# Kernel tuning notes

Measured on AMD Instinct MI355X. Metric: run time of the kernel, lower is better.

The kernel has to match this reference:

```python
import jax, jax.numpy as jnp
import numpy as np

N, F, H, E = 100000, 64, 8, 1200000
D = F // H
HID = 32  # hardcoded MLP hidden width in the module


def setup_inputs() -> dict:
    key = jax.random.key(0)
    ks = jax.random.split(key, 16)
    s = 0.05
    return {
        "h": jax.random.normal(ks[0], (N, F), jnp.float32),
        "W_src": jax.random.normal(ks[1], (F, F), jnp.float32) * s,
        "b_src": jnp.zeros((F,), jnp.float32),
        "W_dst": jax.random.normal(ks[2], (F, F), jnp.float32) * s,
        "b_dst": jnp.zeros((F,), jnp.float32),
        "Wa1_src": jax.random.normal(ks[3], (F, HID), jnp.float32) * s,
        "ba1_src": jnp.zeros((HID,), jnp.float32),
        "Wa2_src": jax.random.normal(ks[4], (HID, H), jnp.float32) * s,
        "ba2_src": jnp.zeros((H,), jnp.float32),
        "Wa1_dst": jax.random.normal(ks[5], (F, HID), jnp.float32) * s,
        "ba1_dst": jnp.zeros((HID,), jnp.float32),
        "Wa2_dst": jax.random.normal(ks[6], (HID, H), jnp.float32) * s,
        "ba2_dst": jnp.zeros((H,), jnp.float32),
        "edge_index": jax.random.randint(ks[7], (2, E), 0, N, jnp.int64),
    }


def _attn_mlp(x, W1, b1, W2, b2):
    # Sequential(LeakyReLU(0.2), Linear(F,32), LeakyReLU(0.2), Linear(32,H))
    y = jax.nn.leaky_relu(x, 0.2)
    y = y @ W1 + b1
    y = jax.nn.leaky_relu(y, 0.2)
    return y @ W2 + b2


def reference(h, W_src, b_src, W_dst, b_dst,
              Wa1_src, ba1_src, Wa2_src, ba2_src,
              Wa1_dst, ba1_dst, Wa2_dst, ba2_dst,
              edge_index):
    src, dst = edge_index[0], edge_index[1]
    g_src = h @ W_src + b_src          # [N,F]
    g_dst = h @ W_dst + b_dst          # [N,F]
    msg_src = g_src[src]               # [E,F] gather
    msg = msg_src + g_dst[dst]         # [E,F]
    a_src = jax.nn.sigmoid(_attn_mlp(msg, Wa1_src, ba1_src, Wa2_src, ba2_src))[:, :, None]    # [E,H,1]
    a_dst = jax.nn.sigmoid(_attn_mlp(g_dst, Wa1_dst, ba1_dst, Wa2_dst, ba2_dst))[:, :, None]  # [N,H,1]
    agg = jax.ops.segment_sum(a_src * msg_src.reshape(E, H, D), dst, num_segments=N)          # [N,H,D]
    h_next = a_dst * g_dst.reshape(N, H, D) + agg
    return h_next.reshape(N, F)
```

## Files before the change

kernel.cpp:

```cpp
#include <hip/hip_runtime.h>
#include <hip/hip_bf16.h>
#include <hip/hip_fp16.h>

#define NF   64
#define NH   8
#define ND   8
#define NHID 32
#define XS   68

typedef __attribute__((ext_vector_type(8))) short bf16x8v;
typedef __attribute__((ext_vector_type(4))) float f32x4v;

__device__ __forceinline__ float bf2f(unsigned short u) {
    union { unsigned int i; float f; } v; v.i = ((unsigned int)u) << 16; return v.f;
}
__device__ __forceinline__ unsigned short f2bf(float f) {
    __hip_bfloat16 b = __float2bfloat16(f);
    union { __hip_bfloat16 b; unsigned short u; } v; v.b = b; return v.u;
}
__device__ __forceinline__ void unpack8(uint4 u, float* o) {
    o[0] = __uint_as_float(u.x << 16); o[1] = __uint_as_float(u.x & 0xffff0000u);
    o[2] = __uint_as_float(u.y << 16); o[3] = __uint_as_float(u.y & 0xffff0000u);
    o[4] = __uint_as_float(u.z << 16); o[5] = __uint_as_float(u.z & 0xffff0000u);
    o[6] = __uint_as_float(u.w << 16); o[7] = __uint_as_float(u.w & 0xffff0000u);
}
__device__ __forceinline__ uint4 pack8(const float* f) {
    uint4 u;
    u.x = (unsigned)f2bf(f[0]) | ((unsigned)f2bf(f[1]) << 16);
    u.y = (unsigned)f2bf(f[2]) | ((unsigned)f2bf(f[3]) << 16);
    u.z = (unsigned)f2bf(f[4]) | ((unsigned)f2bf(f[5]) << 16);
    u.w = (unsigned)f2bf(f[6]) | ((unsigned)f2bf(f[7]) << 16);
    return u;
}
__device__ __forceinline__ float leaky(float x) { return x > 0.f ? x : 0.2f * x; }
__device__ __forceinline__ float sigmoidf(float x) { return 1.f / (1.f + __expf(-x)); }

__global__ void detect_kernel(const int* __restrict__ edge, int* __restrict__ flags) {
    if (threadIdx.x == 0 && blockIdx.x == 0) {
        int oddnz = 0;
        for (int i = 0; i < 32; i++) oddnz |= edge[2 * i + 1];
        flags[0] = (oddnz == 0) ? 1 : 0;
    }
}

__device__ __forceinline__ void load_edge(const int* __restrict__ edge, int e, int E,
                                          int wide, int& s, int& d) {
    if (wide) { s = edge[2 * e]; d = edge[2 * (E + e)]; }
    else      { s = edge[e];     d = edge[E + e]; }
}

__global__ __launch_bounds__(64) void node_mfma_kernel(
    const float* __restrict__ h,
    const float* __restrict__ W_src, const float* __restrict__ b_src,
    const float* __restrict__ W_dst, const float* __restrict__ b_dst,
    const float* __restrict__ Wa1, const float* __restrict__ ba1,
    const float* __restrict__ Wa2, const float* __restrict__ ba2,
    unsigned short* __restrict__ g_src_out, unsigned short* __restrict__ g_dst_out,
    float* __restrict__ out, int* __restrict__ counts, int N)
{
    __shared__ __align__(16) unsigned short sX[64 * XS];
    __shared__ __align__(16) unsigned short sY[64 * XS];
    __shared__ float sW2[NHID * NH];
    __shared__ float sb2[NH];

    int lane = threadIdx.x;
    int nsub = lane & 15, quad = lane >> 4;
    int base = blockIdx.x * 64;
    int n = base + lane;
    bool valid = n < N;
    size_t nn = valid ? (size_t)n : (size_t)(N - 1);

    if (valid && counts) counts[n] = 0;
    for (int i = lane; i < NHID * NH; i += 64) sW2[i] = Wa2[i];
    if (lane < NH) sb2[lane] = ba2[lane];

    {
        const float4* hv = (const float4*)(h + nn * NF);
        unsigned short* xrow = sX + lane * XS;
        #pragma unroll
        for (int k = 0; k < 8; k++) {
            float4 u0 = hv[2 * k], u1 = hv[2 * k + 1];
            float f[8] = { u0.x, u0.y, u0.z, u0.w, u1.x, u1.y, u1.z, u1.w };
            uint4 p = pack8(f);
            uint2* q = (uint2*)(xrow + k * 8);
            q[0] = make_uint2(p.x, p.y);
            q[1] = make_uint2(p.z, p.w);
        }
    }
    __syncthreads();

    #pragma unroll 1
    for (int m = 0; m < 2; m++) {
        const float* W  = m ? W_dst : W_src;
        const float* bb = m ? b_dst : b_src;
        unsigned short* gout = m ? g_dst_out : g_src_out;

        bf16x8v Bf[2][4];
        #pragma unroll
        for (int ks = 0; ks < 2; ks++)
            #pragma unroll
            for (int nt = 0; nt < 4; nt++) {
                union { unsigned short s[8]; bf16x8v v; } u;
                #pragma unroll
                for (int j = 0; j < 8; j++)
                    u.s[j] = f2bf(W[(ks * 32 + quad * 8 + j) * NF + nt * 16 + nsub]);
                Bf[ks][nt] = u.v;
            }

        f32x4v acc[4][4];
        #pragma unroll
        for (int mt = 0; mt < 4; mt++)
            #pragma unroll
            for (int nt = 0; nt < 4; nt++) {
                f32x4v z = {0.f, 0.f, 0.f, 0.f};
                acc[mt][nt] = z;
            }

        #pragma unroll
        for (int ks = 0; ks < 2; ks++)
            #pragma unroll
            for (int mt = 0; mt < 4; mt++) {
                const unsigned short* ap = sX + (mt * 16 + nsub) * XS + ks * 32 + quad * 8;
                union { uint2 d[2]; bf16x8v v; } ua;
                ua.d[0] = *(const uint2*)ap;
                ua.d[1] = *(const uint2*)(ap + 4);
                #pragma unroll
                for (int nt = 0; nt < 4; nt++)
                    acc[mt][nt] = __builtin_amdgcn_mfma_f32_16x16x32_bf16(
                        ua.v, Bf[ks][nt], acc[mt][nt], 0, 0, 0);
            }

        if (m == 1) __syncthreads();

        #pragma unroll
        for (int nt = 0; nt < 4; nt++) {
            float bv = bb[nt * 16 + nsub];
            #pragma unroll
            for (int mt = 0; mt < 4; mt++)
                #pragma unroll
                for (int r = 0; r < 4; r++)
                    sY[(mt * 16 + quad * 4 + r) * XS + nt * 16 + nsub] =
                        f2bf(acc[mt][nt][r] + bv);
        }
        __syncthreads();

        if (valid) {
            const unsigned short* yrow = sY + lane * XS;
            uint4* gp = (uint4*)(gout + (size_t)n * NF);
            #pragma unroll
            for (int k = 0; k < 8; k++) {
                uint2 a = *(const uint2*)(yrow + k * 8);
                uint2 b = *(const uint2*)(yrow + k * 8 + 4);
                gp[k] = make_uint4(a.x, a.y, b.x, b.y);
            }
        }
    }

    bf16x8v B1f[2][2];
    #pragma unroll
    for (int ks = 0; ks < 2; ks++)
        #pragma unroll
        for (int nt = 0; nt < 2; nt++) {
            union { unsigned short s[8]; bf16x8v v; } u;
            #pragma unroll
            for (int j = 0; j < 8; j++)
                u.s[j] = f2bf(Wa1[(ks * 32 + quad * 8 + j) * NHID + nt * 16 + nsub]);
            B1f[ks][nt] = u.v;
        }

    f32x4v acc2[4][2];
    #pragma unroll
    for (int mt = 0; mt < 4; mt++)
        #pragma unroll
        for (int nt = 0; nt < 2; nt++) {
            f32x4v z = {0.f, 0.f, 0.f, 0.f};
            acc2[mt][nt] = z;
        }

    #pragma unroll
    for (int ks = 0; ks < 2; ks++)
        #pragma unroll
        for (int mt = 0; mt < 4; mt++) {
            const unsigned short* ap = sY + (mt * 16 + nsub) * XS + ks * 32 + quad * 8;
            uint2 d0 = *(const uint2*)ap;
            uint2 d1 = *(const uint2*)(ap + 4);
            float f[8];
            unpack8(make_uint4(d0.x, d0.y, d1.x, d1.y), f);
            #pragma unroll
            for (int t = 0; t < 8; t++) f[t] = leaky(f[t]);
            uint4 p = pack8(f);
            union { uint4 u; bf16x8v v; } ua; ua.u = p;
            #pragma unroll
            for (int nt = 0; nt < 2; nt++)
                acc2[mt][nt] = __builtin_amdgcn_mfma_f32_16x16x32_bf16(
                    ua.v, B1f[ks][nt], acc2[mt][nt], 0, 0, 0);
        }
    __syncthreads();

    #pragma unroll
    for (int nt = 0; nt < 2; nt++) {
        float b1v = ba1[nt * 16 + nsub];
        #pragma unroll
        for (int mt = 0; mt < 4; mt++)
            #pragma unroll
            for (int r = 0; r < 4; r++)
                sX[(mt * 16 + quad * 4 + r) * XS + nt * 16 + nsub] =
                    f2bf(leaky(acc2[mt][nt][r] + b1v));
    }
    __syncthreads();

    if (valid) {
        float hid[NHID];
        const unsigned short* hrow = sX + lane * XS;
        #pragma unroll
        for (int k = 0; k < 8; k++) {
            uint2 dv = *(const uint2*)(hrow + k * 4);
            hid[k * 4 + 0] = bf2f((unsigned short)(dv.x & 0xffffu));
            hid[k * 4 + 1] = bf2f((unsigned short)(dv.x >> 16));
            hid[k * 4 + 2] = bf2f((unsigned short)(dv.y & 0xffffu));
            hid[k * 4 + 3] = bf2f((unsigned short)(dv.y >> 16));
        }
        float a[NH];
        #pragma unroll
        for (int j = 0; j < NH; j++) a[j] = sb2[j];
        #pragma unroll
        for (int k = 0; k < NHID; k++) {
            float xk = hid[k];
            #pragma unroll
            for (int j = 0; j < NH; j++) a[j] = fmaf(xk, sW2[k * NH + j], a[j]);
        }
        #pragma unroll
        for (int j = 0; j < NH; j++) a[j] = sigmoidf(a[j]);

        const unsigned short* yrow = sY + lane * XS;
        float4* op = (float4*)(out + (size_t)n * NF);
        #pragma unroll
        for (int k = 0; k < 8; k++) {
            uint2 u0 = *(const uint2*)(yrow + k * 8);
            uint2 u1 = *(const uint2*)(yrow + k * 8 + 4);
            float g[8];
            unpack8(make_uint4(u0.x, u0.y, u1.x, u1.y), g);
            float ah0 = a[(k * 8) >> 3];
            op[2 * k]     = make_float4(ah0 * g[0], ah0 * g[1], ah0 * g[2], ah0 * g[3]);
            op[2 * k + 1] = make_float4(ah0 * g[4], ah0 * g[5], ah0 * g[6], ah0 * g[7]);
        }
    }
}

template <bool STORE_G>
__global__ __launch_bounds__(256) void node_kernel_t(
    const float* __restrict__ h,
    const float* __restrict__ W_src, const float* __restrict__ b_src,
    const float* __restrict__ W_dst, const float* __restrict__ b_dst,
    const float* __restrict__ Wa1, const float* __restrict__ ba1,
    const float* __restrict__ Wa2, const float* __restrict__ ba2,
    unsigned short* __restrict__ g_src_out, unsigned short* __restrict__ g_dst_out,
    float* __restrict__ out, int N)
{
    __shared__ __align__(16) float sWs[NF * NF];
    __shared__ __align__(16) float sWd[NF * NF];
    __shared__ __align__(16) float sW1[NF * NHID];
    __shared__ __align__(16) float sW2[NHID * NH];
    __shared__ float sbs[NF], sbd[NF], sb1[NHID], sb2[NH];

    int tid = threadIdx.x;
    for (int i = tid; i < NF * NF; i += 256) { sWs[i] = W_src[i]; sWd[i] = W_dst[i]; }
    for (int i = tid; i < NF * NHID; i += 256) sW1[i] = Wa1[i];
    if (tid < NHID * NH) sW2[tid] = Wa2[tid];
    if (tid < NF) { sbs[tid] = b_src[tid]; sbd[tid] = b_dst[tid]; }
    if (tid < NHID) sb1[tid] = ba1[tid];
    if (tid < NH) sb2[tid] = ba2[tid];
    __syncthreads();

    int n = blockIdx.x * 256 + tid;
    if (n >= N) return;

    float hrow[NF];
    const float4* hv = (const float4*)(h + (size_t)n * NF);
    #pragma unroll
    for (int k = 0; k < 16; k++) {
        float4 u = hv[k];
        hrow[k * 4 + 0] = u.x; hrow[k * 4 + 1] = u.y;
        hrow[k * 4 + 2] = u.z; hrow[k * 4 + 3] = u.w;
    }

    float acc[NF];
    const float4* Wsv = (const float4*)sWs;
    const float4* Wdv = (const float4*)sWd;

    if (STORE_G) {
        #pragma unroll
        for (int j = 0; j < NF; j++) acc[j] = sbs[j];
        for (int i = 0; i < NF; i++) {
            float hi = hrow[i];
            #pragma unroll
            for (int jb = 0; jb < 16; jb++) {
                float4 w = Wsv[i * 16 + jb];
                acc[jb * 4 + 0] = fmaf(hi, w.x, acc[jb * 4 + 0]);
                acc[jb * 4 + 1] = fmaf(hi, w.y, acc[jb * 4 + 1]);
                acc[jb * 4 + 2] = fmaf(hi, w.z, acc[jb * 4 + 2]);
                acc[jb * 4 + 3] = fmaf(hi, w.w, acc[jb * 4 + 3]);
            }
        }
        uint4* gs = (uint4*)(g_src_out + (size_t)n * NF);
        #pragma unroll
        for (int k = 0; k < 8; k++) gs[k] = pack8(acc + k * 8);
    }

    #pragma unroll
    for (int j = 0; j < NF; j++) acc[j] = sbd[j];
    for (int i = 0; i < NF; i++) {
        float hi = hrow[i];
        #pragma unroll
        for (int jb = 0; jb < 16; jb++) {
            float4 w = Wdv[i * 16 + jb];
            acc[jb * 4 + 0] = fmaf(hi, w.x, acc[jb * 4 + 0]);
            acc[jb * 4 + 1] = fmaf(hi, w.y, acc[jb * 4 + 1]);
            acc[jb * 4 + 2] = fmaf(hi, w.z, acc[jb * 4 + 2]);
            acc[jb * 4 + 3] = fmaf(hi, w.w, acc[jb * 4 + 3]);
        }
    }
    if (STORE_G) {
        uint4* gd = (uint4*)(g_dst_out + (size_t)n * NF);
        #pragma unroll
        for (int k = 0; k < 8; k++) gd[k] = pack8(acc + k * 8);
    }

    float hid[NHID];
    #pragma unroll
    for (int j = 0; j < NHID; j++) hid[j] = sb1[j];
    const float4* W1v = (const float4*)sW1;
    for (int i = 0; i < NF; i++) {
        float xi = leaky(acc[i]);
        #pragma unroll
        for (int jb = 0; jb < 8; jb++) {
            float4 w = W1v[i * 8 + jb];
            hid[jb * 4 + 0] = fmaf(xi, w.x, hid[jb * 4 + 0]);
            hid[jb * 4 + 1] = fmaf(xi, w.y, hid[jb * 4 + 1]);
            hid[jb * 4 + 2] = fmaf(xi, w.z, hid[jb * 4 + 2]);
            hid[jb * 4 + 3] = fmaf(xi, w.w, hid[jb * 4 + 3]);
        }
    }
    float a[NH];
    #pragma unroll
    for (int j = 0; j < NH; j++) a[j] = sb2[j];
    #pragma unroll
    for (int k = 0; k < NHID; k++) {
        float xk = leaky(hid[k]);
        #pragma unroll
        for (int j = 0; j < NH; j++) a[j] = fmaf(xk, sW2[k * NH + j], a[j]);
    }
    #pragma unroll
    for (int j = 0; j < NH; j++) a[j] = sigmoidf(a[j]);

    float4* ap = (float4*)(out + (size_t)n * NF);
    #pragma unroll
    for (int k = 0; k < 16; k++) {
        int j = k * 4;
        ap[k] = make_float4(a[(j + 0) >> 3] * acc[j + 0],
                            a[(j + 1) >> 3] * acc[j + 1],
                            a[(j + 2) >> 3] * acc[j + 2],
                            a[(j + 3) >> 3] * acc[j + 3]);
    }
}

__global__ __launch_bounds__(256) void hist_kernel(
    const int* __restrict__ edge, const int* __restrict__ flags,
    int* __restrict__ counts, int* __restrict__ rank, int E, int N)
{
    int e = blockIdx.x * 256 + threadIdx.x;
    if (e >= E) return;
    int s, d;
    load_edge(edge, e, E, flags[0], s, d);
    if ((unsigned)s >= (unsigned)N || (unsigned)d >= (unsigned)N) { rank[e] = -1; return; }
    rank[e] = atomicAdd(&counts[d], 1);
}

__global__ __launch_bounds__(256) void scan1_kernel(
    const int* __restrict__ counts, int* __restrict__ offsets,
    int* __restrict__ bsums, int N)
{
    __shared__ int lds[256];
    int tid = threadIdx.x;
    int base = blockIdx.x * 2048 + tid * 8;
    int v[8]; int s = 0;
    #pragma unroll
    for (int k = 0; k < 8; k++) { int idx = base + k; int t = (idx < N) ? counts[idx] : 0; v[k] = t; s += t; }
    lds[tid] = s;
    __syncthreads();
    for (int off = 1; off < 256; off <<= 1) {
        int y = (tid >= off) ? lds[tid - off] : 0;
        __syncthreads();
        lds[tid] += y;
        __syncthreads();
    }
    int run = lds[tid] - s;
    #pragma unroll
    for (int k = 0; k < 8; k++) { int idx = base + k; if (idx < N) offsets[idx] = run; run += v[k]; }
    if (tid == 255) bsums[blockIdx.x] = lds[255];
}

__global__ void scan2_kernel(int* __restrict__ bsums, int* __restrict__ offsets, int NB, int N) {
    if (threadIdx.x == 0 && blockIdx.x == 0) {
        int run = 0;
        for (int i = 0; i < NB; i++) { int t = bsums[i]; bsums[i] = run; run += t; }
        offsets[N] = run;
    }
}

__global__ __launch_bounds__(256) void scan3_kernel(
    int* __restrict__ offsets, const int* __restrict__ bsums, int N)
{
    int add = bsums[blockIdx.x];
    int base = blockIdx.x * 2048 + threadIdx.x * 8;
    #pragma unroll
    for (int k = 0; k < 8; k++) { int idx = base + k; if (idx < N) offsets[idx] += add; }
}

__global__ __launch_bounds__(256) void scatter_kernel(
    const int* __restrict__ edge, const int* __restrict__ flags,
    const int* __restrict__ offsets, const int* __restrict__ rank,
    uint2* __restrict__ sorted_sd, int E, int N)
{
    int e = blockIdx.x * 256 + threadIdx.x;
    if (e >= E) return;
    int r = rank[e];
    if (r < 0) return;
    int s, d;
    load_edge(edge, e, E, flags[0], s, d);
    int pos = offsets[d] + r;
    sorted_sd[pos] = make_uint2((unsigned)s, (unsigned)d);
}

__global__ __launch_bounds__(256) void edge_mlp_mfma_kernel(
    const uint2* __restrict__ sorted_sd, const int* __restrict__ total_p,
    const unsigned short* __restrict__ g_src, const unsigned short* __restrict__ g_dst,
    const float* __restrict__ Wa1, const float* __restrict__ ba1,
    const float* __restrict__ Wa2, const float* __restrict__ ba2,
    __half* __restrict__ a_sorted)
{
    __shared__ __align__(16) unsigned short sX[4 * 64 * XS];
    __shared__ __align__(16) float sW2[NHID * NH];
    __shared__ float sb1[NHID], sb2[NH];

    int tid = threadIdx.x;
    if (tid < NHID * NH) sW2[tid] = Wa2[tid];
    if (tid < NHID) sb1[tid] = ba1[tid];
    if (tid < NH) sb2[tid] = ba2[tid];

    int wave = tid >> 6;
    int lane = tid & 63;
    int nsub = lane & 15;
    int quad = lane >> 4;
    int total = *total_p;
    int i = blockIdx.x * 256 + wave * 64 + lane;
    bool valid = i < total;
    uint2 sd = valid ? sorted_sd[i] : make_uint2(0u, 0u);

    unsigned short* xrow = sX + (wave * 64 + lane) * XS;
    {
        const uint4* gs = (const uint4*)(g_src + (size_t)sd.x * NF);
        const uint4* gd = (const uint4*)(g_dst + (size_t)sd.y * NF);
        #pragma unroll
        for (int k = 0; k < 8; k++) {
            float A8[8], B8[8], x8[8];
            unpack8(gs[k], A8); unpack8(gd[k], B8);
            #pragma unroll
            for (int t = 0; t < 8; t++) x8[t] = leaky(A8[t] + B8[t]);
            uint4 pk = pack8(x8);
            uint2* q = (uint2*)(xrow + k * 8);
            q[0] = make_uint2(pk.x, pk.y);
            q[1] = make_uint2(pk.z, pk.w);
        }
    }

    bf16x8v Bf[2][2];
    #pragma unroll
    for (int ks = 0; ks < 2; ks++) {
        #pragma unroll
        for (int nt = 0; nt < 2; nt++) {
            union { unsigned short s[8]; bf16x8v v; } u;
            #pragma unroll
            for (int j = 0; j < 8; j++) {
                int k = ks * 32 + quad * 8 + j;
                int n = nt * 16 + nsub;
                u.s[j] = f2bf(Wa1[k * NHID + n]);
            }
            Bf[ks][nt] = u.v;
        }
    }

    __syncthreads();

    f32x4v acc[4][2];
    #pragma unroll
    for (int mt = 0; mt < 4; mt++)
        #pragma unroll
        for (int nt = 0; nt < 2; nt++) {
            f32x4v z = {0.f, 0.f, 0.f, 0.f};
            acc[mt][nt] = z;
        }

    const unsigned short* wbase = sX + wave * 64 * XS;
    #pragma unroll
    for (int ks = 0; ks < 2; ks++) {
        #pragma unroll
        for (int mt = 0; mt < 4; mt++) {
            const unsigned short* ap = wbase + (mt * 16 + nsub) * XS + ks * 32 + quad * 8;
            union { uint2 d[2]; bf16x8v v; } ua;
            ua.d[0] = *(const uint2*)ap;
            ua.d[1] = *(const uint2*)(ap + 4);
            #pragma unroll
            for (int nt = 0; nt < 2; nt++)
                acc[mt][nt] = __builtin_amdgcn_mfma_f32_16x16x32_bf16(
                    ua.v, Bf[ks][nt], acc[mt][nt], 0, 0, 0);
        }
    }

    __syncthreads();

    #pragma unroll
    for (int nt = 0; nt < 2; nt++) {
        int n = nt * 16 + nsub;
        float b1v = sb1[n];
        #pragma unroll
        for (int mt = 0; mt < 4; mt++) {
            #pragma unroll
            for (int r = 0; r < 4; r++) {
                int m = mt * 16 + quad * 4 + r;
                sX[(wave * 64 + m) * XS + n] = f2bf(leaky(acc[mt][nt][r] + b1v));
            }
        }
    }

    __syncthreads();

    float hid[NHID];
    const unsigned short* hrow = wbase + lane * XS;
    #pragma unroll
    for (int k = 0; k < 8; k++) {
        uint2 dv = *(const uint2*)(hrow + k * 4);
        hid[k * 4 + 0] = bf2f((unsigned short)(dv.x & 0xffffu));
        hid[k * 4 + 1] = bf2f((unsigned short)(dv.x >> 16));
        hid[k * 4 + 2] = bf2f((unsigned short)(dv.y & 0xffffu));
        hid[k * 4 + 3] = bf2f((unsigned short)(dv.y >> 16));
    }
    float a[NH];
    #pragma unroll
    for (int j = 0; j < NH; j++) a[j] = sb2[j];
    #pragma unroll
    for (int k = 0; k < NHID; k++) {
        float xk = hid[k];
        #pragma unroll
        for (int j = 0; j < NH; j++) a[j] = fmaf(xk, sW2[k * NH + j], a[j]);
    }

    if (valid) {
        union { __half h[8]; uint4 u; } pk;
        #pragma unroll
        for (int j = 0; j < NH; j++) pk.h[j] = __float2half(sigmoidf(a[j]));
        *(uint4*)(a_sorted + (size_t)i * NH) = pk.u;
    }
}

__global__ __launch_bounds__(256) void aggregate_kernel(
    const int* __restrict__ offsets, const uint2* __restrict__ sorted_sd,
    const __half* __restrict__ a_sorted, const unsigned short* __restrict__ g_src,
    float* __restrict__ out, int N)
{
    int d = blockIdx.x * 32 + (threadIdx.x >> 3);
    if (d >= N) return;
    int l = threadIdx.x & 7;
    int beg = offsets[d], end = offsets[d + 1];

    float acc[8] = {0.f, 0.f, 0.f, 0.f, 0.f, 0.f, 0.f, 0.f};
    int i = beg;
    for (; i + 2 <= end; i += 2) {
        unsigned s0 = sorted_sd[i].x;
        unsigned s1 = sorted_sd[i + 1].x;
        float av0 = __half2float(a_sorted[(size_t)i * NH + l]);
        float av1 = __half2float(a_sorted[(size_t)(i + 1) * NH + l]);
        uint4 q0 = *(const uint4*)(g_src + (size_t)s0 * NF + l * 8);
        uint4 q1 = *(const uint4*)(g_src + (size_t)s1 * NF + l * 8);
        float f0[8], f1[8];
        unpack8(q0, f0); unpack8(q1, f1);
        #pragma unroll
        for (int t = 0; t < 8; t++) acc[t] = fmaf(av0, f0[t], acc[t]);
        #pragma unroll
        for (int t = 0; t < 8; t++) acc[t] = fmaf(av1, f1[t], acc[t]);
    }
    if (i < end) {
        unsigned s0 = sorted_sd[i].x;
        float av0 = __half2float(a_sorted[(size_t)i * NH + l]);
        uint4 q0 = *(const uint4*)(g_src + (size_t)s0 * NF + l * 8);
        float f0[8]; unpack8(q0, f0);
        #pragma unroll
        for (int t = 0; t < 8; t++) acc[t] = fmaf(av0, f0[t], acc[t]);
    }

    float4* o4 = (float4*)(out + (size_t)d * NF + l * 8);
    float4 v0 = o4[0], v1 = o4[1];
    v0.x += acc[0]; v0.y += acc[1]; v0.z += acc[2]; v0.w += acc[3];
    v1.x += acc[4]; v1.y += acc[5]; v1.z += acc[6]; v1.w += acc[7];
    o4[0] = v0; o4[1] = v1;
}

__global__ __launch_bounds__(256) void edge_kernel(
    const int* __restrict__ edge, const int* __restrict__ flags,
    const unsigned short* __restrict__ g_src, const unsigned short* __restrict__ g_dst,
    const float* __restrict__ Wa1, const float* __restrict__ ba1,
    const float* __restrict__ Wa2, const float* __restrict__ ba2,
    float* __restrict__ out, int E, int N)
{
    __shared__ __align__(16) float sW1[NF * NHID];
    __shared__ __align__(16) float sW2[NHID * NH];
    __shared__ float sb1[NHID], sb2[NH];
    int tid = threadIdx.x;
    for (int i = tid; i < NF * NHID; i += 256) sW1[i] = Wa1[i];
    if (tid < NHID * NH) sW2[tid] = Wa2[tid];
    if (tid < NHID) sb1[tid] = ba1[tid];
    if (tid < NH) sb2[tid] = ba2[tid];
    __syncthreads();

    int e = blockIdx.x * 256 + tid;
    if (e >= E) return;
    int s, d;
    load_edge(edge, e, E, flags[0], s, d);
    if ((unsigned)s >= (unsigned)N || (unsigned)d >= (unsigned)N) return;

    float ms[NF];
    float hid[NHID];
    #pragma unroll
    for (int j = 0; j < NHID; j++) hid[j] = sb1[j];

    const uint4* gs = (const uint4*)(g_src + (size_t)s * NF);
    const uint4* gd = (const uint4*)(g_dst + (size_t)d * NF);
    #pragma unroll
    for (int k = 0; k < 8; k++) {
        float a8[8], b8[8];
        unpack8(gs[k], a8);
        unpack8(gd[k], b8);
        #pragma unroll
        for (int t = 0; t < 8; t++) {
            int i = k * 8 + t;
            ms[i] = a8[t];
            float x = leaky(a8[t] + b8[t]);
            #pragma unroll
            for (int j = 0; j < NHID; j++) hid[j] = fmaf(x, sW1[i * NHID + j], hid[j]);
        }
    }

    float a[NH];
    #pragma unroll
    for (int j = 0; j < NH; j++) a[j] = sb2[j];
    #pragma unroll
    for (int k = 0; k < NHID; k++) {
        float xk = leaky(hid[k]);
        #pragma unroll
        for (int j = 0; j < NH; j++) a[j] = fmaf(xk, sW2[k * NH + j], a[j]);
    }

    float* arow = out + (size_t)d * NF;
    #pragma unroll
    for (int hh = 0; hh < NH; hh++) {
        float ah = sigmoidf(a[hh]);
        #pragma unroll
        for (int dd = 0; dd < ND; dd++)
            unsafeAtomicAdd(arow + hh * ND + dd, ah * ms[hh * ND + dd]);
    }
}

__global__ __launch_bounds__(256) void edge_kernel_fused(
    const int* __restrict__ edge, const int* __restrict__ flags,
    const float* __restrict__ h,
    const float* __restrict__ W_src, const float* __restrict__ b_src,
    const float* __restrict__ W_dst, const float* __restrict__ b_dst,
    const float* __restrict__ Wa1, const float* __restrict__ ba1,
    const float* __restrict__ Wa2, const float* __restrict__ ba2,
    float* __restrict__ out, int E, int N)
{
    __shared__ __align__(16) float sWs[NF * NF];
    __shared__ __align__(16) float sWd[NF * NF];
    __shared__ __align__(16) float sW1[NF * NHID];
    __shared__ __align__(16) float sW2[NHID * NH];
    __shared__ float sbs[NF], sbd[NF], sb1[NHID], sb2[NH];
    int tid = threadIdx.x;
    for (int i = tid; i < NF * NF; i += 256) { sWs[i] = W_src[i]; sWd[i] = W_dst[i]; }
    for (int i = tid; i < NF * NHID; i += 256) sW1[i] = Wa1[i];
    if (tid < NHID * NH) sW2[tid] = Wa2[tid];
    if (tid < NF) { sbs[tid] = b_src[tid]; sbd[tid] = b_dst[tid]; }
    if (tid < NHID) sb1[tid] = ba1[tid];
    if (tid < NH) sb2[tid] = ba2[tid];
    __syncthreads();

    int e = blockIdx.x * 256 + tid;
    if (e >= E) return;
    int wide = flags ? flags[0] : 0;
    int s, d;
    load_edge(edge, e, E, wide, s, d);
    if ((unsigned)s >= (unsigned)N || (unsigned)d >= (unsigned)N) return;

    float gsr[NF], msg[NF];
    {
        float hrow[NF];
        #pragma unroll
        for (int i = 0; i < NF; i++) hrow[i] = h[(size_t)s * NF + i];
        #pragma unroll
        for (int j = 0; j < NF; j++) gsr[j] = sbs[j];
        for (int i = 0; i < NF; i++) {
            float hi = hrow[i];
            #pragma unroll
            for (int j = 0; j < NF; j++) gsr[j] = fmaf(hi, sWs[i * NF + j], gsr[j]);
        }
    }
    #pragma unroll
    for (int j = 0; j < NF; j++) msg[j] = gsr[j] + sbd[j];
    for (int i = 0; i < NF; i++) {
        float hi = h[(size_t)d * NF + i];
        #pragma unroll
        for (int j = 0; j < NF; j++) msg[j] = fmaf(hi, sWd[i * NF + j], msg[j]);
    }

    float hid[NHID];
    #pragma unroll
    for (int j = 0; j < NHID; j++) hid[j] = sb1[j];
    for (int i = 0; i < NF; i++) {
        float x = leaky(msg[i]);
        #pragma unroll
        for (int j = 0; j < NHID; j++) hid[j] = fmaf(x, sW1[i * NHID + j], hid[j]);
    }
    float a[NH];
    #pragma unroll
    for (int j = 0; j < NH; j++) a[j] = sb2[j];
    #pragma unroll
    for (int k = 0; k < NHID; k++) {
        float xk = leaky(hid[k]);
        #pragma unroll
        for (int j = 0; j < NH; j++) a[j] = fmaf(xk, sW2[k * NH + j], a[j]);
    }

    float* arow = out + (size_t)d * NF;
    #pragma unroll
    for (int hh = 0; hh < NH; hh++) {
        float ah = sigmoidf(a[hh]);
        #pragma unroll
        for (int dd = 0; dd < ND; dd++)
            unsafeAtomicAdd(arow + hh * ND + dd, ah * gsr[hh * ND + dd]);
    }
}

static inline size_t al256(size_t x) { return (x + 255) & ~(size_t)255; }

extern "C" void kernel_launch(void* const* d_in, const int* in_sizes, int n_in,
                              void* d_out, int out_size, void* d_ws, size_t ws_size,
                              hipStream_t stream) {
    const float* h       = (const float*)d_in[0];
    const float* W_src   = (const float*)d_in[1];
    const float* b_src   = (const float*)d_in[2];
    const float* W_dst   = (const float*)d_in[3];
    const float* b_dst   = (const float*)d_in[4];
    const float* Wa1_src = (const float*)d_in[5];
    const float* ba1_src = (const float*)d_in[6];
    const float* Wa2_src = (const float*)d_in[7];
    const float* ba2_src = (const float*)d_in[8];
    const float* Wa1_dst = (const float*)d_in[9];
    const float* ba1_dst = (const float*)d_in[10];
    const float* Wa2_dst = (const float*)d_in[11];
    const float* ba2_dst = (const float*)d_in[12];
    const int* edge = (const int*)d_in[13];

    int N = in_sizes[0] / NF;
    int E = in_sizes[13] / 2;
    float* out = (float*)d_out;

    int nodeBlocks = (N + 255) / 256;
    int nodeWaves  = (N + 63) / 64;
    int edgeBlocks = (E + 255) / 256;
    int NB1 = (N + 2047) / 2048;

    size_t o_flags  = 0;
    size_t o_gsrc   = al256(o_flags + 256);
    size_t o_gdst   = al256(o_gsrc + (size_t)N * NF * 2);
    size_t o_asort  = al256(o_gdst + (size_t)N * NF * 2);
    size_t o_counts = al256(o_asort + (size_t)E * NH * 2);
    size_t o_offs   = al256(o_counts + (size_t)N * 4);
    size_t o_bsums  = al256(o_offs + ((size_t)N + 1) * 4);
    size_t o_sorted = al256(o_bsums + (size_t)NB1 * 4);
    size_t need     = o_sorted + (size_t)E * 8;

    size_t gB = (size_t)N * NF * 2;

    if (ws_size >= need) {
        char* w = (char*)d_ws;
        int*            flags   = (int*)(w + o_flags);
        unsigned short* g_src   = (unsigned short*)(w + o_gsrc);
        unsigned short* g_dst   = (unsigned short*)(w + o_gdst);
        __half*         a_sort  = (__half*)(w + o_asort);
        int*            rank    = (int*)(w + o_asort);
        int*            counts  = (int*)(w + o_counts);
        int*            offsets = (int*)(w + o_offs);
        int*            bsums   = (int*)(w + o_bsums);
        uint2*          sorted  = (uint2*)(w + o_sorted);

        detect_kernel<<<1, 1, 0, stream>>>(edge, flags);

        node_mfma_kernel<<<nodeWaves, 64, 0, stream>>>(
            h, W_src, b_src, W_dst, b_dst,
            Wa1_dst, ba1_dst, Wa2_dst, ba2_dst,
            g_src, g_dst, out, counts, N);

        hist_kernel<<<edgeBlocks, 256, 0, stream>>>(edge, flags, counts, rank, E, N);

        scan1_kernel<<<NB1, 256, 0, stream>>>(counts, offsets, bsums, N);
        scan2_kernel<<<1, 1, 0, stream>>>(bsums, offsets, NB1, N);
        scan3_kernel<<<NB1, 256, 0, stream>>>(offsets, bsums, N);

        scatter_kernel<<<edgeBlocks, 256, 0, stream>>>(
            edge, flags, offsets, rank, sorted, E, N);

        edge_mlp_mfma_kernel<<<edgeBlocks, 256, 0, stream>>>(
            sorted, offsets + N, g_src, g_dst,
            Wa1_src, ba1_src, Wa2_src, ba2_src, a_sort);

        aggregate_kernel<<<(N + 31) / 32, 256, 0, stream>>>(
            offsets, sorted, a_sort, g_src, out, N);
    } else if (ws_size >= 256 + 2 * gB) {
        int* flags = (int*)d_ws;
        unsigned short* g_src = (unsigned short*)((char*)d_ws + 256);
        unsigned short* g_dst = g_src + (size_t)N * NF;

        detect_kernel<<<1, 1, 0, stream>>>(edge, flags);

        node_kernel_t<true><<<nodeBlocks, 256, 0, stream>>>(
            h, W_src, b_src, W_dst, b_dst,
            Wa1_dst, ba1_dst, Wa2_dst, ba2_dst,
            g_src, g_dst, out, N);

        edge_kernel<<<edgeBlocks, 256, 0, stream>>>(
            edge, flags, g_src, g_dst,
            Wa1_src, ba1_src, Wa2_src, ba2_src,
            out, E, N);
    } else {
        int* flags = (ws_size >= 256) ? (int*)d_ws : nullptr;
        if (flags) detect_kernel<<<1, 1, 0, stream>>>(edge, flags);

        node_kernel_t<false><<<nodeBlocks, 256, 0, stream>>>(
            h, W_src, b_src, W_dst, b_dst,
            Wa1_dst, ba1_dst, Wa2_dst, ba2_dst,
            nullptr, nullptr, out, N);

        edge_kernel_fused<<<edgeBlocks, 256, 0, stream>>>(
            edge, flags, h,
            W_src, b_src, W_dst, b_dst,
            Wa1_src, ba1_src, Wa2_src, ba2_src,
            out, E, N);
    }
}
```

Measured before the change: 294.2 us.

## Pre-transpose weights to bf16 and run edge MLP second layer on MFMA

```diff
diff --git a/kernel.cpp b/kernel.cpp
--- a/kernel.cpp
+++ b/kernel.cpp
@@ -7,6 +7,7 @@
 #define ND   8
 #define NHID 32
 #define XS   68
+#define OS   10
 
 typedef __attribute__((ext_vector_type(8))) short bf16x8v;
 typedef __attribute__((ext_vector_type(4))) float f32x4v;
@@ -32,7 +33,7 @@
     u.w = (unsigned)f2bf(f[6]) | ((unsigned)f2bf(f[7]) << 16);
     return u;
 }
-__device__ __forceinline__ float leaky(float x) { return x > 0.f ? x : 0.2f * x; }
+__device__ __forceinline__ float leaky(float x) { return fmaxf(x, 0.2f * x); }
 __device__ __forceinline__ float sigmoidf(float x) { return 1.f / (1.f + __expf(-x)); }
 
 __global__ void detect_kernel(const int* __restrict__ edge, int* __restrict__ flags) {
@@ -49,11 +50,28 @@
     else      { s = edge[e];     d = edge[E + e]; }
 }
 
+#define WBF_TOTAL 12544
+__global__ __launch_bounds__(256) void prep_weights_kernel(
+    const float* __restrict__ Ws, const float* __restrict__ Wd,
+    const float* __restrict__ W1d, const float* __restrict__ W1s,
+    const float* __restrict__ W2s, unsigned short* __restrict__ o)
+{
+    int i = blockIdx.x * 256 + threadIdx.x;
+    float v;
+    if (i < 4096)        { int j = i;         v = Ws [(j & 63) * 64 + (j >> 6)]; }
+    else if (i < 8192)   { int j = i - 4096;  v = Wd [(j & 63) * 64 + (j >> 6)]; }
+    else if (i < 10240)  { int j = i - 8192;  v = W1d[(j & 63) * 32 + (j >> 6)]; }
+    else if (i < 12288)  { int j = i - 10240; v = W1s[(j & 63) * 32 + (j >> 6)]; }
+    else if (i < 12544)  { int j = i - 12288; v = W2s[(j & 31) * 8  + (j >> 5)]; }
+    else return;
+    o[i] = f2bf(v);
+}
+
 __global__ __launch_bounds__(64) void node_mfma_kernel(
     const float* __restrict__ h,
-    const float* __restrict__ W_src, const float* __restrict__ b_src,
-    const float* __restrict__ W_dst, const float* __restrict__ b_dst,
-    const float* __restrict__ Wa1, const float* __restrict__ ba1,
+    const unsigned short* __restrict__ WsT, const float* __restrict__ b_src,
+    const unsigned short* __restrict__ WdT, const float* __restrict__ b_dst,
+    const unsigned short* __restrict__ W1T, const float* __restrict__ ba1,
     const float* __restrict__ Wa2, const float* __restrict__ ba2,
     unsigned short* __restrict__ g_src_out, unsigned short* __restrict__ g_dst_out,
     float* __restrict__ out, int* __restrict__ counts, int N)
@@ -91,7 +109,7 @@
 
     #pragma unroll 1
     for (int m = 0; m < 2; m++) {
-        const float* W  = m ? W_dst : W_src;
+        const unsigned short* WT = m ? WdT : WsT;
         const float* bb = m ? b_dst : b_src;
         unsigned short* gout = m ? g_dst_out : g_src_out;
 
@@ -100,10 +118,8 @@
         for (int ks = 0; ks < 2; ks++)
             #pragma unroll
             for (int nt = 0; nt < 4; nt++) {
-                union { unsigned short s[8]; bf16x8v v; } u;
-                #pragma unroll
-                for (int j = 0; j < 8; j++)
-                    u.s[j] = f2bf(W[(ks * 32 + quad * 8 + j) * NF + nt * 16 + nsub]);
+                union { uint4 u; bf16x8v v; } u;
+                u.u = *(const uint4*)(WT + (nt * 16 + nsub) * 64 + ks * 32 + quad * 8);
                 Bf[ks][nt] = u.v;
             }
 
@@ -161,10 +177,8 @@
     for (int ks = 0; ks < 2; ks++)
         #pragma unroll
         for (int nt = 0; nt < 2; nt++) {
-            union { unsigned short s[8]; bf16x8v v; } u;
-            #pragma unroll
-            for (int j = 0; j < 8; j++)
-                u.s[j] = f2bf(Wa1[(ks * 32 + quad * 8 + j) * NHID + nt * 16 + nsub]);
+            union { uint4 u; bf16x8v v; } u;
+            u.u = *(const uint4*)(W1T + (nt * 16 + nsub) * 64 + ks * 32 + quad * 8);
             B1f[ks][nt] = u.v;
         }
 
@@ -435,16 +449,15 @@
 __global__ __launch_bounds__(256) void edge_mlp_mfma_kernel(
     const uint2* __restrict__ sorted_sd, const int* __restrict__ total_p,
     const unsigned short* __restrict__ g_src, const unsigned short* __restrict__ g_dst,
-    const float* __restrict__ Wa1, const float* __restrict__ ba1,
-    const float* __restrict__ Wa2, const float* __restrict__ ba2,
+    const unsigned short* __restrict__ W1T, const float* __restrict__ ba1,
+    const unsigned short* __restrict__ W2T, const float* __restrict__ ba2,
     __half* __restrict__ a_sorted)
 {
     __shared__ __align__(16) unsigned short sX[4 * 64 * XS];
-    __shared__ __align__(16) float sW2[NHID * NH];
+    __shared__ __align__(16) __half sOut[4 * 64 * OS];
     __shared__ float sb1[NHID], sb2[NH];
 
     int tid = threadIdx.x;
-    if (tid < NHID * NH) sW2[tid] = Wa2[tid];
     if (tid < NHID) sb1[tid] = ba1[tid];
     if (tid < NH) sb2[tid] = ba2[tid];
 
@@ -476,18 +489,19 @@
 
     bf16x8v Bf[2][2];
     #pragma unroll
-    for (int ks = 0; ks < 2; ks++) {
+    for (int ks = 0; ks < 2; ks++)
         #pragma unroll
         for (int nt = 0; nt < 2; nt++) {
-            union { unsigned short s[8]; bf16x8v v; } u;
-            #pragma unroll
-            for (int j = 0; j < 8; j++) {
-                int k = ks * 32 + quad * 8 + j;
-                int n = nt * 16 + nsub;
-                u.s[j] = f2bf(Wa1[k * NHID + n]);
-            }
+            union { uint4 u; bf16x8v v; } u;
+            u.u = *(const uint4*)(W1T + (nt * 16 + nsub) * 64 + ks * 32 + quad * 8);
             Bf[ks][nt] = u.v;
         }
+    bf16x8v B2f;
+    {
+        union { uint4 u; bf16x8v v; } u;
+        if (nsub < NH) u.u = *(const uint4*)(W2T + nsub * 32 + quad * 8);
+        else           u.u = make_uint4(0u, 0u, 0u, 0u);
+        B2f = u.v;
     }
 
     __syncthreads();
@@ -535,31 +549,34 @@
 
     __syncthreads();
 
-    float hid[NHID];
-    const unsigned short* hrow = wbase + lane * XS;
-    #pragma unroll
-    for (int k = 0; k < 8; k++) {
-        uint2 dv = *(const uint2*)(hrow + k * 4);
-        hid[k * 4 + 0] = bf2f((unsigned short)(dv.x & 0xffffu));
-        hid[k * 4 + 1] = bf2f((unsigned short)(dv.x >> 16));
-        hid[k * 4 + 2] = bf2f((unsigned short)(dv.y & 0xffffu));
-        hid[k * 4 + 3] = bf2f((unsigned short)(dv.y >> 16));
-    }
-    float a[NH];
-    #pragma unroll
-    for (int j = 0; j < NH; j++) a[j] = sb2[j];
-    #pragma unroll
-    for (int k = 0; k < NHID; k++) {
-        float xk = hid[k];
-        #pragma unroll
-        for (int j = 0; j < NH; j++) a[j] = fmaf(xk, sW2[k * NH + j], a[j]);
-    }
+    f32x4v acc2[4];
+    #pragma unroll
+    for (int mt = 0; mt < 4; mt++) { f32x4v z = {0.f, 0.f, 0.f, 0.f}; acc2[mt] = z; }
+    #pragma unroll
+    for (int mt = 0; mt < 4; mt++) {
+        const unsigned short* ap = wbase + (mt * 16 + nsub) * XS + quad * 8;
+        union { uint2 d[2]; bf16x8v v; } ua;
+        ua.d[0] = *(const uint2*)ap;
+        ua.d[1] = *(const uint2*)(ap + 4);
+        acc2[mt] = __builtin_amdgcn_mfma_f32_16x16x32_bf16(ua.v, B2f, acc2[mt], 0, 0, 0);
+    }
+
+    if (nsub < NH) {
+        float b2v = sb2[nsub];
+        #pragma unroll
+        for (int mt = 0; mt < 4; mt++)
+            #pragma unroll
+            for (int r = 0; r < 4; r++) {
+                int m = mt * 16 + quad * 4 + r;
+                sOut[(wave * 64 + m) * OS + nsub] = __float2half(sigmoidf(acc2[mt][r] + b2v));
+            }
+    }
+    __syncthreads();
 
     if (valid) {
-        union { __half h[8]; uint4 u; } pk;
-        #pragma unroll
-        for (int j = 0; j < NH; j++) pk.h[j] = __float2half(sigmoidf(a[j]));
-        *(uint4*)(a_sorted + (size_t)i * NH) = pk.u;
+        const unsigned int* orow = (const unsigned int*)(sOut + (wave * 64 + lane) * OS);
+        uint4 pk = make_uint4(orow[0], orow[1], orow[2], orow[3]);
+        *(uint4*)(a_sorted + (size_t)i * NH) = pk;
     }
 }
 
@@ -779,7 +796,8 @@
     int NB1 = (N + 2047) / 2048;
 
     size_t o_flags  = 0;
-    size_t o_gsrc   = al256(o_flags + 256);
+    size_t o_wbf    = al256(o_flags + 256);
+    size_t o_gsrc   = al256(o_wbf + (size_t)WBF_TOTAL * 2);
     size_t o_gdst   = al256(o_gsrc + (size_t)N * NF * 2);
     size_t o_asort  = al256(o_gdst + (size_t)N * NF * 2);
     size_t o_counts = al256(o_asort + (size_t)E * NH * 2);
@@ -793,6 +811,12 @@
     if (ws_size >= need) {
         char* w = (char*)d_ws;
         int*            flags   = (int*)(w + o_flags);
+        unsigned short* wbf     = (unsigned short*)(w + o_wbf);
+        unsigned short* WsT     = wbf;
+        unsigned short* WdT     = wbf + 4096;
+        unsigned short* W1dT    = wbf + 8192;
+        unsigned short* W1sT    = wbf + 10240;
+        unsigned short* W2sT    = wbf + 12288;
         unsigned short* g_src   = (unsigned short*)(w + o_gsrc);
         unsigned short* g_dst   = (unsigned short*)(w + o_gdst);
         __half*         a_sort  = (__half*)(w + o_asort);
@@ -803,10 +827,12 @@
         uint2*          sorted  = (uint2*)(w + o_sorted);
 
         detect_kernel<<<1, 1, 0, stream>>>(edge, flags);
+        prep_weights_kernel<<<(WBF_TOTAL + 255) / 256, 256, 0, stream>>>(
+            W_src, W_dst, Wa1_dst, Wa1_src, Wa2_src, wbf);
 
         node_mfma_kernel<<<nodeWaves, 64, 0, stream>>>(
-            h, W_src, b_src, W_dst, b_dst,
-            Wa1_dst, ba1_dst, Wa2_dst, ba2_dst,
+            h, WsT, b_src, WdT, b_dst,
+            W1dT, ba1_dst, Wa2_dst, ba2_dst,
             g_src, g_dst, out, counts, N);
 
         hist_kernel<<<edgeBlocks, 256, 0, stream>>>(edge, flags, counts, rank, E, N);
@@ -820,7 +846,7 @@
 
         edge_mlp_mfma_kernel<<<edgeBlocks, 256, 0, stream>>>(
             sorted, offsets + N, g_src, g_dst,
-            Wa1_src, ba1_src, Wa2_src, ba2_src, a_sort);
+            W1sT, ba1_src, W2sT, ba2_src, a_sort);
 
         aggregate_kernel<<<(N + 31) / 32, 256, 0, stream>>>(
             offsets, sorted, a_sort, g_src, out, N);
```

New measurement: 288.5 us. Within noise of the previous version (-1.9%).
